# Optimization experiments

Measured on AMD Instinct MI355X. Metric: run time of the kernel, lower is better.

Reference implementation:

```python
import jax, jax.numpy as jnp
import numpy as np


def setup_inputs() -> dict:
    key = jax.random.key(0)
    ks = jax.random.split(key, 10)
    B, L, D_MODEL = 2, 2048, 1024
    D_INNER, N, W, R = 2048, 16, 4, 64
    s = 0.02
    return {
        "hidden_states": jax.random.normal(ks[0], (B, L, D_MODEL), jnp.float32),
        "in_proj_w": jax.random.normal(ks[1], (2 * D_INNER, D_MODEL), jnp.float32) * s,
        "conv_w": jax.random.normal(ks[2], (D_INNER, W), jnp.float32) * 0.2,
        "conv_b": jax.random.normal(ks[3], (D_INNER,), jnp.float32) * 0.02,
        "x_proj_w": jax.random.normal(ks[4], (R + 2 * N, D_INNER), jnp.float32) * s,
        "dt_proj_w": jax.random.normal(ks[5], (D_INNER, R), jnp.float32) * (R ** -0.5),
        "dt_proj_b": jnp.log(jnp.expm1(jnp.exp(jax.random.uniform(ks[6], (D_INNER,), jnp.float32, np.log(1e-3), np.log(1e-1)))) + 1e-20),
        "A_log": jnp.log(jnp.broadcast_to(jnp.arange(1, N + 1, dtype=jnp.float32), (D_INNER, N))),
        "D_param": jnp.ones((D_INNER,), jnp.float32),
        "out_proj_w": jax.random.normal(ks[7], (D_MODEL, D_INNER), jnp.float32) * s,
    }


def _mamba_fwd(hidden_states, in_proj_w, conv_w, conv_b, x_proj_w,
               dt_proj_w, dt_proj_b, A_log, D_param, out_proj_w):
    Bsz, L, _ = hidden_states.shape
    d_inner = conv_w.shape[0]
    n = A_log.shape[1]
    r = dt_proj_w.shape[1]

    # input projection -> x, z  (each [B, L, d_inner])
    xz = jnp.einsum('bld,ed->ble', hidden_states, in_proj_w)
    x, z = xz[..., :d_inner], xz[..., d_inner:]

    # depthwise causal conv over L with SiLU
    x_bdl = jnp.transpose(x, (0, 2, 1))  # [B, d, L]
    kern = conv_w[:, None, :]            # [d, 1, W]
    xc = jax.lax.conv_general_dilated(
        x_bdl, kern, window_strides=(1,), padding=[(conv_w.shape[1] - 1, 0)],
        dimension_numbers=('NCH', 'OIH', 'NCH'), feature_group_count=d_inner)
    xc = xc + conv_b[None, :, None]
    xc = xc * jax.nn.sigmoid(xc)         # silu, [B, d, L]
    u = jnp.transpose(xc, (0, 2, 1))     # [B, L, d]

    # SSM parameter projections
    x_dbl = jnp.einsum('bld,ed->ble', u, x_proj_w)   # [B, L, r+2n]
    dt_lo = x_dbl[..., :r]
    B_ssm = x_dbl[..., r:r + n]                       # [B, L, n]
    C_ssm = x_dbl[..., r + n:]                        # [B, L, n]
    delta = jax.nn.softplus(jnp.einsum('blr,dr->bld', dt_lo, dt_proj_w) + dt_proj_b)

    A = -jnp.exp(A_log)  # [d, n]

    # selective scan over time (sequential recurrence)
    def step(h, inp):
        d_t, u_t, b_t, c_t = inp  # [B,d], [B,d], [B,n], [B,n]
        dA = jnp.exp(d_t[..., None] * A)                       # [B,d,n]
        h = dA * h + (d_t * u_t)[..., None] * b_t[:, None, :]  # [B,d,n]
        y_t = jnp.einsum('bdn,bn->bd', h, c_t)
        return h, y_t

    h0 = jnp.zeros((Bsz, d_inner, n), dtype=u.dtype)
    xs = (jnp.transpose(delta, (1, 0, 2)), jnp.transpose(u, (1, 0, 2)),
          jnp.transpose(B_ssm, (1, 0, 2)), jnp.transpose(C_ssm, (1, 0, 2)))
    _, ys = jax.lax.scan(step, h0, xs)           # ys: [L, B, d]
    y = jnp.transpose(ys, (1, 0, 2)) + u * D_param
    y = y * (z * jax.nn.sigmoid(z))              # gate: y * silu(z)
    return jnp.einsum('bld,ed->ble', y, out_proj_w)


def reference(hidden_states, in_proj_w, conv_w, conv_b, x_proj_w,
              dt_proj_w, dt_proj_b, A_log, D_param, out_proj_w):
    return _mamba_fwd(hidden_states, in_proj_w, conv_w, conv_b, x_proj_w,
                      dt_proj_w, dt_proj_b, A_log, D_param, out_proj_w)
```

## Files before the change

### kernel.cpp

```cpp
#include <hip/hip_runtime.h>
#include <cstdint>
#include <cstddef>

#define Bsz  2
#define Lseq 2048
#define DM   1024
#define DI   2048
#define NS   16
#define RR   64
#define BL   (Bsz * Lseq)
#define TC   64
#define NC   (Lseq / TC)

typedef unsigned short u16;
typedef __attribute__((ext_vector_type(4))) unsigned short u16x4;
typedef __attribute__((ext_vector_type(8))) short short8;
typedef __attribute__((ext_vector_type(4))) float f32x4;

__device__ __forceinline__ u16 f32_to_bf16(float f) {
  union { float f; unsigned int u; } v; v.f = f;
  unsigned int lsb = (v.u >> 16) & 1u;
  v.u += 0x7fffu + lsb;
  return (u16)(v.u >> 16);
}
__device__ __forceinline__ float bf16_to_f32(u16 h) {
  union { unsigned int u; float f; } v; v.u = ((unsigned int)h) << 16;
  return v.f;
}

__global__ void cvt_f32_bf16(const float* __restrict__ src, u16* __restrict__ dst, int n) {
  int i = (blockIdx.x * blockDim.x + threadIdx.x) * 4;
  if (i + 4 <= n) {
    float4 v = *(const float4*)(src + i);
    dst[i + 0] = f32_to_bf16(v.x);
    dst[i + 1] = f32_to_bf16(v.y);
    dst[i + 2] = f32_to_bf16(v.z);
    dst[i + 3] = f32_to_bf16(v.w);
  } else {
    for (; i < n; ++i) dst[i] = f32_to_bf16(src[i]);
  }
}

__global__ void split_bf16_kernel(const float* __restrict__ src,
                                  u16* __restrict__ hi, u16* __restrict__ lo, int n) {
  int i = blockIdx.x * blockDim.x + threadIdx.x;
  if (i >= n) return;
  const float v = src[i];
  const u16 h = f32_to_bf16(v);
  hi[i] = h;
  lo[i] = f32_to_bf16(v - bf16_to_f32(h));
}

__device__ __forceinline__ void gload_lds16(const u16* g, u16* l) {
  __builtin_amdgcn_global_load_lds(
      (const __attribute__((address_space(1))) unsigned int*)g,
      (__attribute__((address_space(3))) unsigned int*)l,
      16, 0, 0);
}

template<bool BF16OUT>
__global__ __launch_bounds__(256) void gemm128_bt(
    const u16* __restrict__ A, const u16* __restrict__ Bt,
    void* __restrict__ outA_, void* __restrict__ outB_,
    int split, int ldA, int ldB, int K, int kstride, size_t zstride)
{
  __shared__ __align__(16) u16 As[128 * 32];
  __shared__ __align__(16) u16 Bs[128 * 32];
  const int tid  = threadIdx.x;
  const int lane = tid & 63;
  const int wid  = tid >> 6;

  const int nwg = gridDim.x * gridDim.y;
  int wg = blockIdx.y * gridDim.x + blockIdx.x;
  wg = (wg & 7) * (nwg >> 3) + (wg >> 3);
  const int m0 = (wg / gridDim.x) * 128;
  const int n0 = (wg % gridDim.x) * 128;
  const int kbase = blockIdx.z * K;

  const int wr = wid >> 1, wc = wid & 1;

  const f32x4 zero = {0.f, 0.f, 0.f, 0.f};
  f32x4 acc[4][4];
#pragma unroll
  for (int i = 0; i < 4; ++i)
#pragma unroll
    for (int j = 0; j < 4; ++j) acc[i][j] = zero;

  const int l16 = lane * 16;

  for (int k0 = 0; k0 < K; k0 += 32) {
    __syncthreads();
#pragma unroll
    for (int c = 0; c < 2; ++c) {
      const int base = c * 4096 + wid * 1024;
      const int ofs  = base + l16;
      const int row  = ofs >> 6;
      const int col  = (ofs >> 1) & 31;
      gload_lds16(A  + (size_t)(m0 + row) * kstride + kbase + k0 + col, (u16*)((char*)As + base));
      gload_lds16(Bt + (size_t)(n0 + row) * kstride + kbase + k0 + col, (u16*)((char*)Bs + base));
    }
    __syncthreads();

    const int kk = (lane >> 4) * 8;
    const int ra = wr * 64 + (lane & 15);
    const int rb = wc * 64 + (lane & 15);
    short8 af[4], bf[4];
#pragma unroll
    for (int i = 0; i < 4; ++i) af[i] = *(const short8*)&As[(ra + i * 16) * 32 + kk];
#pragma unroll
    for (int j = 0; j < 4; ++j) bf[j] = *(const short8*)&Bs[(rb + j * 16) * 32 + kk];
#pragma unroll
    for (int i = 0; i < 4; ++i)
#pragma unroll
      for (int j = 0; j < 4; ++j)
        acc[i][j] = __builtin_amdgcn_mfma_f32_16x16x32_bf16(af[i], bf[j], acc[i][j], 0, 0, 0);
  }

  const bool isA = (n0 < split);
  const int  ld  = isA ? ldA : ldB;
  const int  nb  = isA ? n0 : n0 - split;
  const int cr = (lane >> 4) * 4;
  const int cc = lane & 15;
  if constexpr (BF16OUT) {
    u16* o = (u16*)(isA ? outA_ : outB_);
#pragma unroll
    for (int i = 0; i < 4; ++i)
#pragma unroll
      for (int j = 0; j < 4; ++j)
#pragma unroll
        for (int r = 0; r < 4; ++r) {
          const int m = m0 + wr * 64 + i * 16 + cr + r;
          const int n = nb + wc * 64 + j * 16 + cc;
          o[(size_t)m * ld + n] = f32_to_bf16(acc[i][j][r]);
        }
  } else {
    float* o = (float*)(isA ? outA_ : outB_) + (size_t)blockIdx.z * zstride;
#pragma unroll
    for (int i = 0; i < 4; ++i)
#pragma unroll
      for (int j = 0; j < 4; ++j)
#pragma unroll
        for (int r = 0; r < 4; ++r) {
          const int m = m0 + wr * 64 + i * 16 + cr + r;
          const int n = nb + wc * 64 + j * 16 + cc;
          o[(size_t)m * ld + n] = acc[i][j][r];
        }
  }
}

__global__ void add2_kernel(const float* __restrict__ part, float* __restrict__ out) {
  const int i = (blockIdx.x * blockDim.x + threadIdx.x) * 4;
  const float4 a = *(const float4*)(part + i);
  const float4 b = *(const float4*)(part + (size_t)BL * DM + i);
  float4 s;
  s.x = a.x + b.x; s.y = a.y + b.y; s.z = a.z + b.z; s.w = a.w + b.w;
  *(float4*)(out + i) = s;
}

__global__ __launch_bounds__(256) void gemm_xproj(
    const u16* __restrict__ A, const u16* __restrict__ Bt,
    float* __restrict__ xdbl, u16* __restrict__ dhi, u16* __restrict__ dlo)
{
  const int wg   = blockIdx.x * 4 + (threadIdx.x >> 6);
  const int lane = threadIdx.x & 63;
  const int mt = wg / 6, nt = wg % 6;

  const u16* arow = A  + (size_t)(mt * 16 + (lane & 15)) * DI + ((lane >> 4) * 8);
  const u16* brow = Bt + (size_t)(nt * 16 + (lane & 15)) * DI + ((lane >> 4) * 8);
  f32x4 acc = {0.f, 0.f, 0.f, 0.f};
  for (int k0 = 0; k0 < DI; k0 += 32) {
    short8 a = *(const short8*)(arow + k0);
    short8 b = *(const short8*)(brow + k0);
    acc = __builtin_amdgcn_mfma_f32_16x16x32_bf16(a, b, acc, 0, 0, 0);
  }
  const int cr = (lane >> 4) * 4, cc = lane & 15;
  const int n  = nt * 16 + cc;
#pragma unroll
  for (int r = 0; r < 4; ++r) {
    const int m = mt * 16 + cr + r;
    const float v = acc[r];
    if (n < RR) {
      const u16 h = f32_to_bf16(v);
      dhi[(size_t)m * RR + n] = h;
      dlo[(size_t)m * RR + n] = f32_to_bf16(v - bf16_to_f32(h));
    } else {
      xdbl[(size_t)m * 96 + n] = v;
    }
  }
}

__global__ __launch_bounds__(256) void dt_gemm_mfma(
    const u16* __restrict__ ahi, const u16* __restrict__ alo,
    const u16* __restrict__ bhi, const u16* __restrict__ blo,
    const float* __restrict__ dtb, float* __restrict__ delta)
{
  const int wg   = blockIdx.x * 4 + (threadIdx.x >> 6);
  const int lane = threadIdx.x & 63;
  const int mt = wg >> 7, nt = wg & 127;

  const size_t aofs = (size_t)(mt * 16 + (lane & 15)) * 64 + ((lane >> 4) * 8);
  const size_t bofs = (size_t)(nt * 16 + (lane & 15)) * 64 + ((lane >> 4) * 8);

  f32x4 acc = {0.f, 0.f, 0.f, 0.f};
#pragma unroll
  for (int k0 = 0; k0 < 64; k0 += 32) {
    const short8 Ah = *(const short8*)(ahi + aofs + k0);
    const short8 Al = *(const short8*)(alo + aofs + k0);
    const short8 Bh = *(const short8*)(bhi + bofs + k0);
    const short8 Bl = *(const short8*)(blo + bofs + k0);
    acc = __builtin_amdgcn_mfma_f32_16x16x32_bf16(Ah, Bh, acc, 0, 0, 0);
    acc = __builtin_amdgcn_mfma_f32_16x16x32_bf16(Ah, Bl, acc, 0, 0, 0);
    acc = __builtin_amdgcn_mfma_f32_16x16x32_bf16(Al, Bh, acc, 0, 0, 0);
  }

  const int cr = (lane >> 4) * 4, cc = lane & 15;
  const int n  = nt * 16 + cc;
  const float b = dtb[n];
#pragma unroll
  for (int r = 0; r < 4; ++r) {
    const float s = acc[r] + b;
    const float sp = fmaxf(s, 0.f) + __logf(1.f + __expf(-fabsf(s)));
    delta[(size_t)(mt * 16 + cr + r) * DI + n] = sp;
  }
}

__global__ void conv_silu_kernel(const u16* __restrict__ x,
                                 const float* __restrict__ cw, const float* __restrict__ cb,
                                 u16* __restrict__ ub)
{
  const int idx  = blockIdx.x * blockDim.x + threadIdx.x;
  const int base = idx * 4;
  const int d  = base & (DI - 1);
  const int bl = base >> 11;
  const int l  = bl & (Lseq - 1);
  const u16* xp = x + (size_t)bl * DI + d;
  const u16x4 zv = {0, 0, 0, 0};
  const u16x4 x3 = *(const u16x4*)xp;
  const u16x4 x2 = (l >= 1) ? *(const u16x4*)(xp - DI)     : zv;
  const u16x4 x1 = (l >= 2) ? *(const u16x4*)(xp - 2 * DI) : zv;
  const u16x4 x0 = (l >= 3) ? *(const u16x4*)(xp - 3 * DI) : zv;
  const float4 bias = *(const float4*)&cb[d];
  u16x4 out;
#pragma unroll
  for (int j = 0; j < 4; ++j) {
    const float4 w = *(const float4*)&cw[(d + j) * 4];
    float acc = ((const float*)&bias)[j];
    acc += bf16_to_f32(x0[j]) * w.x + bf16_to_f32(x1[j]) * w.y +
           bf16_to_f32(x2[j]) * w.z + bf16_to_f32(x3[j]) * w.w;
    const float s = acc / (1.f + __expf(-acc));
    out[j] = f32_to_bf16(s);
  }
  *(u16x4*)(ub + (size_t)bl * DI + d) = out;
}


__global__ __launch_bounds__(256) void scan_chunk_ps(
    const float* __restrict__ delta, const u16* __restrict__ u,
    const float* __restrict__ xdbl, const float* __restrict__ alog,
    float* __restrict__ Pout, float* __restrict__ Sout)
{
  __shared__ float Bl[TC][NS];
  const int b   = blockIdx.z;
  const int c   = blockIdx.y;
  const int d   = blockIdx.x * 256 + threadIdx.x;
  const int tid = threadIdx.x;
  const size_t rowBase = (size_t)b * Lseq + (size_t)c * TC;

  {
    const int row = tid >> 2, c4 = (tid & 3) * 4;
    *(float4*)&Bl[row][c4] = *(const float4*)&xdbl[(rowBase + row) * 96 + RR + c4];
  }
  __syncthreads();

  float A[NS];
#pragma unroll
  for (int n4 = 0; n4 < 4; ++n4) {
    const float4 a4 = *(const float4*)&alog[(size_t)d * NS + n4 * 4];
    A[n4 * 4 + 0] = -__expf(a4.x);
    A[n4 * 4 + 1] = -__expf(a4.y);
    A[n4 * 4 + 2] = -__expf(a4.z);
    A[n4 * 4 + 3] = -__expf(a4.w);
  }

  float h[NS], P[NS];
#pragma unroll
  for (int n = 0; n < NS; ++n) { h[n] = 0.f; P[n] = 1.f; }

#pragma unroll 4
  for (int t = 0; t < TC; ++t) {
    const float dt  = delta[(rowBase + t) * DI + d];
    const float ut  = bf16_to_f32(u[(rowBase + t) * DI + d]);
    const float dtu = dt * ut;
#pragma unroll
    for (int n = 0; n < NS; ++n) {
      const float dA = __expf(dt * A[n]);
      P[n] *= dA;
      h[n] = dA * h[n] + dtu * Bl[t][n];
    }
  }

  const size_t base = (size_t)(b * NC + c) * NS * DI + d;
#pragma unroll
  for (int n = 0; n < NS; ++n) {
    Pout[base + (size_t)n * DI] = P[n];
    Sout[base + (size_t)n * DI] = h[n];
  }
}

__global__ __launch_bounds__(256) void scan_combine(
    const float* __restrict__ P, const float* __restrict__ S,
    float* __restrict__ Hin)
{
  const int gid = blockIdx.x * 256 + threadIdx.x;
  const int b   = gid >> 15;
  const int nd  = gid & 32767;
  float h = 0.f;
  for (int c = 0; c < NC; ++c) {
    const size_t o = (size_t)(b * NC + c) * (NS * DI) + nd;
    const float Pc = P[o];
    const float Sc = S[o];
    Hin[o] = h;
    h = Pc * h + Sc;
  }
}

__global__ __launch_bounds__(256) void scan_chunk_y(
    const float* __restrict__ delta, const u16* __restrict__ u,
    const float* __restrict__ xdbl, const float* __restrict__ alog,
    const float* __restrict__ dpar, const u16* __restrict__ z,
    const float* __restrict__ Hin, u16* __restrict__ yb)
{
  __shared__ float Bl[TC][NS];
  __shared__ float Cl[TC][NS];
  const int b   = blockIdx.z;
  const int c   = blockIdx.y;
  const int d   = blockIdx.x * 256 + threadIdx.x;
  const int tid = threadIdx.x;
  const size_t rowBase = (size_t)b * Lseq + (size_t)c * TC;

  {
    const int row = tid >> 2, c4 = (tid & 3) * 4;
    *(float4*)&Bl[row][c4] = *(const float4*)&xdbl[(rowBase + row) * 96 + RR + c4];
    *(float4*)&Cl[row][c4] = *(const float4*)&xdbl[(rowBase + row) * 96 + RR + NS + c4];
  }
  __syncthreads();

  float A[NS];
#pragma unroll
  for (int n4 = 0; n4 < 4; ++n4) {
    const float4 a4 = *(const float4*)&alog[(size_t)d * NS + n4 * 4];
    A[n4 * 4 + 0] = -__expf(a4.x);
    A[n4 * 4 + 1] = -__expf(a4.y);
    A[n4 * 4 + 2] = -__expf(a4.z);
    A[n4 * 4 + 3] = -__expf(a4.w);
  }
  const float Dv = dpar[d];

  float h[NS];
  const size_t sbase = (size_t)(b * NC + c) * NS * DI + d;
#pragma unroll
  for (int n = 0; n < NS; ++n) h[n] = Hin[sbase + (size_t)n * DI];

#pragma unroll 4
  for (int t = 0; t < TC; ++t) {
    const float dt  = delta[(rowBase + t) * DI + d];
    const float ut  = bf16_to_f32(u[(rowBase + t) * DI + d]);
    const float zv  = bf16_to_f32(z[(rowBase + t) * DI + d]);
    const float dtu = dt * ut;
    float y = 0.f;
#pragma unroll
    for (int n = 0; n < NS; ++n) {
      const float dA = __expf(dt * A[n]);
      h[n] = dA * h[n] + dtu * Bl[t][n];
      y += h[n] * Cl[t][n];
    }
    const float yv = y + ut * Dv;
    const float g  = zv / (1.f + __expf(-zv));
    yb[(rowBase + t) * DI + d] = f32_to_bf16(yv * g);
  }
}

extern "C" void kernel_launch(void* const* d_in, const int* in_sizes, int n_in,
                              void* d_out, int out_size, void* d_ws, size_t ws_size,
                              hipStream_t stream)
{
  const float* hs   = (const float*)d_in[0];
  const float* win  = (const float*)d_in[1];
  const float* cw   = (const float*)d_in[2];
  const float* cb   = (const float*)d_in[3];
  const float* wxp  = (const float*)d_in[4];
  const float* wdt  = (const float*)d_in[5];
  const float* bdt  = (const float*)d_in[6];
  const float* alog = (const float*)d_in[7];
  const float* dpar = (const float*)d_in[8];
  const float* wout = (const float*)d_in[9];
  float* out = (float*)d_out;

  char* ws = (char*)d_ws;
  size_t off = 0;
  auto alloc = [&](size_t bytes) -> void* {
    void* p = ws + off;
    off += (bytes + 255) & ~(size_t)255;
    return p;
  };
  u16*   hs_b   = (u16*)  alloc((size_t)BL * DM * 2);
  u16*   win_b  = (u16*)  alloc((size_t)2 * DI * DM * 2);
  u16*   wxp_b  = (u16*)  alloc((size_t)96 * DI * 2);
  u16*   wout_b = (u16*)  alloc((size_t)DM * DI * 2);
  u16*   xbuf   = (u16*)  alloc((size_t)BL * DI * 2);
  u16*   zbuf   = (u16*)  alloc((size_t)BL * DI * 2);
  u16*   ub16   = (u16*)  alloc((size_t)BL * DI * 2);
  float* deltab = (float*)alloc((size_t)BL * DI * 4);
  float* xdbl   = (float*)alloc((size_t)BL * 96 * 4);
  float* Pbuf   = (float*)alloc((size_t)Bsz * NC * DI * NS * 4);
  float* Sbuf   = (float*)alloc((size_t)Bsz * NC * DI * NS * 4);
  u16*   dt_hi  = (u16*)  alloc((size_t)BL * 64 * 2);
  u16*   dt_lo  = (u16*)  alloc((size_t)BL * 64 * 2);
  u16*   w_hi   = (u16*)  alloc((size_t)DI * 64 * 2);
  u16*   w_lo   = (u16*)  alloc((size_t)DI * 64 * 2);
  u16*   y_b    = ub16;
  float* Hin    = Pbuf;
  float* part   = deltab;

  const int thr = 256;
  cvt_f32_bf16<<<(BL * DM / 4 + thr - 1) / thr, thr, 0, stream>>>(hs, hs_b, BL * DM);
  cvt_f32_bf16<<<(2 * DI * DM / 4 + thr - 1) / thr, thr, 0, stream>>>(win, win_b, 2 * DI * DM);
  cvt_f32_bf16<<<(96 * DI / 4 + thr - 1) / thr, thr, 0, stream>>>(wxp, wxp_b, 96 * DI);
  cvt_f32_bf16<<<(DM * DI / 4 + thr - 1) / thr, thr, 0, stream>>>(wout, wout_b, DM * DI);
  split_bf16_kernel<<<(DI * 64) / thr, thr, 0, stream>>>(wdt, w_hi, w_lo, DI * 64);

  {
    dim3 g(4096 / 128, BL / 128);
    gemm128_bt<true><<<g, 256, 0, stream>>>(hs_b, win_b, xbuf, zbuf,
                                            DI, DI, DI, DM, DM, 0);
  }

  conv_silu_kernel<<<(BL * DI / 4) / 256, 256, 0, stream>>>(xbuf, cw, cb, ub16);

  gemm_xproj<<<(256 * 6) / 4, 256, 0, stream>>>(ub16, wxp_b, xdbl, dt_hi, dt_lo);

  dt_gemm_mfma<<<(256 * 128) / 4, 256, 0, stream>>>(dt_hi, dt_lo, w_hi, w_lo, bdt, deltab);

  {
    dim3 gA(DI / 256, NC, Bsz);
    scan_chunk_ps<<<gA, 256, 0, stream>>>(deltab, ub16, xdbl, alog, Pbuf, Sbuf);
    scan_combine<<<(Bsz * DI * NS) / 256, 256, 0, stream>>>(Pbuf, Sbuf, Hin);
    scan_chunk_y<<<gA, 256, 0, stream>>>(deltab, ub16, xdbl, alog, dpar, zbuf, Hin, y_b);
  }

  {
    dim3 g(DM / 128, BL / 128, 2);
    gemm128_bt<false><<<g, 256, 0, stream>>>(y_b, wout_b, part, part,
                                             1 << 30, DM, DM, DI / 2, DI,
                                             (size_t)BL * DM);
    add2_kernel<<<(BL * DM / 4) / 256, 256, 0, stream>>>(part, out);
  }
}
```

Baseline: 291.8 us.

## Stage bf16 GEMM epilogue through LDS for vectorized stores; drop workgroup remap

The bf16-output epilogue now writes accumulators into the reused As/Bs shared buffers with an XOR swizzle, in two phases of 64 rows. All threads then read them back and issue 16-byte vector global stores, replacing scattered 2-byte stores. The change also removes the XCD-style workgroup index remapping and uses plain blockIdx tiling, which may reduce L2 locality on a multi-XCD chip. The extra barriers add some synchronization cost.

Result: no change. 294.0 us (+0.7%).

```diff
diff --git a/kernel.cpp b/kernel.cpp
--- a/kernel.cpp
+++ b/kernel.cpp
@@ -14,6 +14,7 @@
 
 typedef unsigned short u16;
 typedef __attribute__((ext_vector_type(4))) unsigned short u16x4;
+typedef __attribute__((ext_vector_type(8))) unsigned short u16x8;
 typedef __attribute__((ext_vector_type(8))) short short8;
 typedef __attribute__((ext_vector_type(4))) float f32x4;
 
@@ -69,12 +70,8 @@
   const int tid  = threadIdx.x;
   const int lane = tid & 63;
   const int wid  = tid >> 6;
-
-  const int nwg = gridDim.x * gridDim.y;
-  int wg = blockIdx.y * gridDim.x + blockIdx.x;
-  wg = (wg & 7) * (nwg >> 3) + (wg >> 3);
-  const int m0 = (wg / gridDim.x) * 128;
-  const int n0 = (wg % gridDim.x) * 128;
+  const int m0 = blockIdx.y * 128;
+  const int n0 = blockIdx.x * 128;
   const int kbase = blockIdx.z * K;
 
   const int wr = wid >> 1, wc = wid & 1;
@@ -121,18 +118,42 @@
   const int  nb  = isA ? n0 : n0 - split;
   const int cr = (lane >> 4) * 4;
   const int cc = lane & 15;
+
   if constexpr (BF16OUT) {
     u16* o = (u16*)(isA ? outA_ : outB_);
 #pragma unroll
-    for (int i = 0; i < 4; ++i)
-#pragma unroll
-      for (int j = 0; j < 4; ++j)
-#pragma unroll
-        for (int r = 0; r < 4; ++r) {
-          const int m = m0 + wr * 64 + i * 16 + cr + r;
-          const int n = nb + wc * 64 + j * 16 + cc;
-          o[(size_t)m * ld + n] = f32_to_bf16(acc[i][j][r]);
+    for (int ph = 0; ph < 2; ++ph) {
+      __syncthreads();
+      if (wr == ph) {
+#pragma unroll
+        for (int i = 0; i < 4; ++i) {
+          u16* lbase = (i < 2) ? As : Bs;
+#pragma unroll
+          for (int r = 0; r < 4; ++r) {
+            const int row  = i * 16 + cr + r;
+            const int lrow = (i < 2) ? row : row - 32;
+            const int sw   = ((row >> 2) & 3) << 4;
+#pragma unroll
+            for (int j = 0; j < 4; ++j) {
+              const int col = wc * 64 + j * 16 + cc;
+              lbase[lrow * 128 + (col ^ sw)] = f32_to_bf16(acc[i][j][r]);
+            }
+          }
         }
+      }
+      __syncthreads();
+#pragma unroll
+      for (int k = 0; k < 4; ++k) {
+        const int linear = tid + k * 256;
+        const int row    = linear >> 4;
+        const int col0   = (linear & 15) * 8;
+        const int sw     = ((row >> 2) & 3) << 4;
+        const u16* src   = (k < 2) ? &As[row * 128 + (col0 ^ sw)]
+                                   : &Bs[(row - 32) * 128 + (col0 ^ sw)];
+        const int m = m0 + ph * 64 + row;
+        *(u16x8*)(o + (size_t)m * ld + nb + col0) = *(const u16x8*)src;
+      }
+    }
   } else {
     float* o = (float*)(isA ? outA_ : outB_) + (size_t)blockIdx.z * zstride;
 #pragma unroll
```
